# Kernel tuning notes

Hardware: AMD Instinct MI355X
Metric: run time of the kernel (lower is better)

Reference implementation:

```python
import jax, jax.numpy as jnp
import numpy as np

# Module constants from Net.__init__
KS = (3, 8, 2)          # kernel_size per pseudo-coordinate dim
K = KS[0] * KS[1] * KS[2]  # 48 spline weight matrices per layer
DIM = 3
S = 2 ** DIM            # 8 nonzero degree-1 B-spline supports per edge
MAX_RADIUS = 4.5
N, E = 20000, 500000


def _glorot(key, shape):
    fan = shape[-2] + shape[-1]
    return jax.random.normal(key, shape, jnp.float32) * jnp.sqrt(2.0 / fan)


def setup_inputs() -> dict:
    key = jax.random.key(0)
    ks = jax.random.split(key, 12)
    x = jax.random.normal(ks[0], (N, 1), jnp.float32)
    edge_index = jax.random.randint(ks[1], (2, E), 0, N)
    # raw pseudo-coordinates in [0, max_radius); normalized inside reference
    pseudo = jax.random.uniform(ks[2], (E, DIM), jnp.float32) * MAX_RADIUS
    return {
        "x": x,
        "edge_index": edge_index,
        "pseudo": pseudo,
        "W1": _glorot(ks[3], (K, 1, 32)),   "root1": _glorot(ks[4], (1, 32)),   "b1": jnp.zeros((32,), jnp.float32),
        "W2": _glorot(ks[5], (K, 32, 64)),  "root2": _glorot(ks[6], (32, 64)),  "b2": jnp.zeros((64,), jnp.float32),
        "W3": _glorot(ks[7], (K, 64, 128)), "root3": _glorot(ks[8], (64, 128)), "b3": jnp.zeros((128,), jnp.float32),
    }


def spline_basis(u):
    """Degree-1 open B-spline basis. u: [E, DIM] in [0,1].
    Returns basis [E, S] and flat kernel indices kidx [E, S] into the K weights."""
    ks_f = jnp.array(KS, jnp.float32)
    pos = u * (ks_f - 1.0)                      # [E, DIM]
    lo = jnp.floor(pos)
    frac = pos - lo                             # interpolation weight per dim
    lo_i = lo.astype(jnp.int32)
    # all 2^DIM corner offsets
    bits = jnp.array([[(s >> d) & 1 for d in range(DIM)] for s in range(S)], jnp.int32)  # [S, DIM]
    idx = jnp.clip(lo_i[:, None, :] + bits[None, :, :], 0, jnp.array(KS, jnp.int32) - 1)  # [E, S, DIM]
    w = jnp.where(bits[None, :, :] == 1, frac[:, None, :], 1.0 - frac[:, None, :])        # [E, S, DIM]
    basis = jnp.prod(w, axis=-1)                # [E, S]
    strides = jnp.array([KS[1] * KS[2], KS[2], 1], jnp.int32)
    kidx = (idx * strides[None, None, :]).sum(-1)  # [E, S]
    return basis, kidx


def spline_conv(x, src, dst, basis, kidx, W, root, bias):
    """SplineGCN layer: gather source features, weight by spline basis,
    scatter-add into per-(node, kernel) buckets, then contract with the K
    kernel matrices. Equivalent to sum_e basis * (x_src @ W[kidx]) at dst."""
    c_in = x.shape[1]
    contrib = basis[:, :, None] * x[src][:, None, :]          # [E, S, c_in]
    flat = (dst[:, None] * K + kidx).reshape(-1)              # [E*S]
    acc = jax.ops.segment_sum(contrib.reshape(-1, c_in), flat, num_segments=N * K)
    acc = acc.reshape(N, K, c_in)                             # [N, K, c_in]
    return jnp.einsum('nki,kio->no', acc, W) + x @ root + bias


def reference(x, edge_index, pseudo, W1, root1, b1, W2, root2, b2, W3, root3, b3):
    u = jnp.clip(pseudo / MAX_RADIUS, 0.0, 1.0)
    basis, kidx = spline_basis(u)
    src, dst = edge_index[0], edge_index[1]
    h = jax.nn.relu(spline_conv(x, src, dst, basis, kidx, W1, root1, b1))
    h = jax.nn.relu(spline_conv(h, src, dst, basis, kidx, W2, root2, b2))
    h = jax.nn.relu(spline_conv(h, src, dst, basis, kidx, W3, root3, b3))
    return jax.nn.log_softmax(h, axis=-1)
```

## Files before the change

kernel.cpp:

```cpp
#include <hip/hip_runtime.h>
#include <hip/hip_bf16.h>

#define NN_NODES 20000
#define NE_EDGES 500000
#define KTOT 48

typedef __bf16 bf16x8 __attribute__((ext_vector_type(8)));
typedef float f32x4 __attribute__((ext_vector_type(4)));

__device__ inline unsigned short bf16_rne(float x) {
    unsigned int u = __float_as_uint(x);
    u = (u + 0x7fffu + ((u >> 16) & 1u)) >> 16;
    return (unsigned short)u;
}

__global__ void zero_kernel(int* __restrict__ p, int n) {
    int i = blockIdx.x * 256 + threadIdx.x;
    if (i < n) p[i] = 0;
}

__global__ void count_kernel(const int* __restrict__ ei, int* __restrict__ counts) {
    int e = blockIdx.x * 256 + threadIdx.x;
    if (e < NE_EDGES) atomicAdd(&counts[ei[NE_EDGES + e]], 1);
}

__global__ void scan_kernel(const int* __restrict__ counts, int* __restrict__ row_start) {
    __shared__ int part[256];
    const int CH = (NN_NODES + 255) / 256;
    int t = threadIdx.x;
    int begin = t * CH;
    int end = begin + CH;
    if (end > NN_NODES) end = NN_NODES;
    int sum = 0;
    for (int i = begin; i < end && i < NN_NODES; ++i) sum += counts[i];
    part[t] = sum;
    __syncthreads();
    for (int off = 1; off < 256; off <<= 1) {
        int v = (t >= off) ? part[t - off] : 0;
        __syncthreads();
        part[t] += v;
        __syncthreads();
    }
    int run = (t == 0) ? 0 : part[t - 1];
    for (int i = begin; i < end && i < NN_NODES; ++i) {
        row_start[i] = run;
        run += counts[i];
    }
    if (t == 255) row_start[NN_NODES] = part[255];
}

__global__ void fill_kernel(const int* __restrict__ ei, const int* __restrict__ row_start,
                            int* __restrict__ cursor, int* __restrict__ slot_pos) {
    int e = blockIdx.x * 256 + threadIdx.x;
    if (e < NE_EDGES) {
        int d = ei[NE_EDGES + e];
        int p = atomicAdd(&cursor[d], 1);
        slot_pos[e] = row_start[d] + p;
    }
}

__global__ void edge_prep_sorted(const float* __restrict__ pseudo, const int* __restrict__ ei,
                                 const int* __restrict__ slot_pos,
                                 int* __restrict__ srcs,
                                 float* __restrict__ bas8, unsigned char* __restrict__ kidb) {
    int e = blockIdx.x * 256 + threadIdx.x;
    if (e >= NE_EDGES) return;
    const int ksa[3] = {3, 8, 2};
    float frac[3];
    int id_lo[3], id_hi[3];
#pragma unroll
    for (int d = 0; d < 3; ++d) {
        float u = pseudo[e * 3 + d] * (1.0f / 4.5f);
        u = fminf(fmaxf(u, 0.0f), 1.0f);
        float pos = u * (float)(ksa[d] - 1);
        float fl = floorf(pos);
        int lo = (int)fl;
        frac[d] = pos - fl;
        id_lo[d] = lo;
        id_hi[d] = (lo + 1 <= ksa[d] - 1) ? lo + 1 : lo - 1;
    }
    int j = slot_pos[e];
    srcs[j] = ei[e];
#pragma unroll
    for (int s = 0; s < 8; ++s) {
        float w = 1.0f;
        int k = 0;
        const int strides[3] = {16, 2, 1};
#pragma unroll
        for (int d = 0; d < 3; ++d) {
            int bit = (s >> d) & 1;
            k += (bit ? id_hi[d] : id_lo[d]) * strides[d];
            w *= bit ? frac[d] : (1.0f - frac[d]);
        }
        bas8[(size_t)j * 8 + s] = w;
        kidb[(size_t)j * 8 + s] = (unsigned char)k;
    }
}

__global__ __launch_bounds__(256) void layer1_fused_kernel(
    const int* __restrict__ srcs, const float* __restrict__ bas8,
    const unsigned char* __restrict__ kidb, const int* __restrict__ row_start,
    const float* __restrict__ x, const float* __restrict__ W1,
    const float* __restrict__ root1, const float* __restrict__ b1,
    unsigned short* __restrict__ h1bf) {
    __shared__ float w1s[KTOT * 32];
    __shared__ float scopy[4][8 * 49];
    int tid = threadIdx.x;
    for (int l = tid; l < KTOT * 32; l += 256) w1s[l] = W1[l];
    int w = tid >> 6, lane = tid & 63;
    int n = blockIdx.x * 4 + w;
    bool act = n < NN_NODES;
    float* sc = &scopy[w][0];
    for (int l = lane; l < 8 * 49; l += 64) sc[l] = 0.0f;
    if (act) {
        int beg = row_start[n], end = row_start[n + 1];
        int es = lane >> 3;
        for (int jb = beg; jb < end; jb += 8) {
            int j = jb + es;
            if (j < end) {
                float b = bas8[(size_t)jb * 8 + lane];
                int k = kidb[(size_t)jb * 8 + lane];
                float xv = x[srcs[j]];
                sc[es * 49 + k] += b * xv;
            }
        }
        if (lane < KTOT) {
            float a = 0.0f;
#pragma unroll
            for (int e = 0; e < 8; ++e) a += sc[e * 49 + lane];
            sc[lane] = a;
        }
    }
    __syncthreads();
    if (act && lane < 32) {
        float s = b1[lane] + x[n] * root1[lane];
#pragma unroll 8
        for (int k = 0; k < KTOT; ++k) s = fmaf(sc[k], w1s[k * 32 + lane], s);
        h1bf[n * 32 + lane] = bf16_rne(fmaxf(s, 0.0f));
    }
}

#define BTSTRIDE 40
template <int CIN>
__global__ __launch_bounds__(256) void mfma_acc_kernel(
    const int* __restrict__ srcs, const float* __restrict__ bas8,
    const unsigned char* __restrict__ kidb, const int* __restrict__ row_start,
    const unsigned short* __restrict__ hbf, unsigned short* __restrict__ abuf,
    int n0, int mc) {
    constexpr int NT = CIN / 16;
    __shared__ unsigned short BtAll[4][KTOT * BTSTRIDE];
    int w = threadIdx.x >> 6, lane = threadIdx.x & 63;
    int n_local = blockIdx.x * 4 + w;
    if (n_local >= mc) return;
    int n = n0 + n_local;
    unsigned short* Bt = &BtAll[w][0];
    int q = lane >> 4;
    int l15 = lane & 15;
    int beg = row_start[n], end = row_start[n + 1];
    int cnt = end - beg;
    f32x4 acc[3][NT] = {};

    for (int c0 = 0; c0 < cnt; c0 += 32) {
        uint4 z = make_uint4(0, 0, 0, 0);
        for (int l = lane; l < (KTOT * BTSTRIDE) / 8; l += 64) ((uint4*)Bt)[l] = z;
#pragma unroll
        for (int it = 0; it < 4; ++it) {
            int idx = it * 64 + lane;
            int jj = idx >> 3, s = idx & 7;
            int j = c0 + jj;
            if (j < cnt) {
                float b = bas8[(size_t)(beg + j) * 8 + s];
                int k = kidb[(size_t)(beg + j) * 8 + s];
                Bt[k * BTSTRIDE + jj] = bf16_rne(b);
            }
        }
        int srcv[8];
#pragma unroll
        for (int j = 0; j < 8; ++j) {
            int jc = c0 + q * 8 + j;
            jc = (jc < cnt) ? jc : (cnt - 1);
            srcv[j] = srcs[beg + jc];
        }
        bf16x8 afr[3];
#pragma unroll
        for (int mt = 0; mt < 3; ++mt) {
            uint4 raw = *(const uint4*)&Bt[(mt * 16 + l15) * BTSTRIDE + q * 8];
            afr[mt] = __builtin_bit_cast(bf16x8, raw);
        }
#pragma unroll
        for (int nt = 0; nt < NT; ++nt) {
            unsigned int bw[4];
#pragma unroll
            for (int jp = 0; jp < 4; ++jp) {
                unsigned int lo = hbf[(size_t)srcv[2 * jp] * CIN + nt * 16 + l15];
                unsigned int hi = hbf[(size_t)srcv[2 * jp + 1] * CIN + nt * 16 + l15];
                bw[jp] = lo | (hi << 16);
            }
            uint4 braw = make_uint4(bw[0], bw[1], bw[2], bw[3]);
            bf16x8 bfr = __builtin_bit_cast(bf16x8, braw);
#pragma unroll
            for (int mt = 0; mt < 3; ++mt)
                acc[mt][nt] = __builtin_amdgcn_mfma_f32_16x16x32_bf16(afr[mt], bfr,
                                                                      acc[mt][nt], 0, 0, 0);
        }
    }

    unsigned short* arow = abuf + (size_t)n_local * (49 * CIN);
#pragma unroll
    for (int mt = 0; mt < 3; ++mt)
#pragma unroll
        for (int nt = 0; nt < NT; ++nt)
#pragma unroll
            for (int r = 0; r < 4; ++r) {
                int kk = mt * 16 + q * 4 + r;
                int ch = nt * 16 + l15;
                arow[kk * CIN + ch] = bf16_rne(acc[mt][nt][r]);
            }
    if (lane < CIN) arow[KTOT * CIN + lane] = hbf[(size_t)n * CIN + lane];
}

__global__ void pack_w_kernel(const float* __restrict__ W, const float* __restrict__ root,
                              int KK, int NN, int total, unsigned short* __restrict__ Wp) {
    int tid = blockIdx.x * 256 + threadIdx.x;
    if (tid >= total) return;
    int nct = NN >> 4;
    int l = tid & 63;
    int c = (tid >> 6) % nct;
    int t = tid / (64 * nct);
    int n = c * 16 + (l & 15);
    int kbase = t * 32 + ((l >> 4) << 3);
    unsigned short vals[8];
#pragma unroll
    for (int jj = 0; jj < 8; ++jj) {
        int k = kbase + jj;
        float v = (k < KK) ? W[(size_t)k * NN + n] : root[(size_t)(k - KK) * NN + n];
        vals[jj] = bf16_rne(v);
    }
    *(uint4*)&Wp[(size_t)tid * 8] = *(uint4*)vals;
}

template <int NCT, int NW, bool LOGSOFTMAX>
__global__ __launch_bounds__(NW * 64) void mfma_gemm_block(
    const unsigned short* __restrict__ A, const unsigned short* __restrict__ Wp,
    const float* __restrict__ bias, void* __restrict__ outp,
    int Kp, int n0, int mc) {
    constexpr int NN = NCT * 16;
    constexpr int RSTR = NN + 2;
    __shared__ float red[NW][16 * RSTR];
    int w = threadIdx.x >> 6, lane = threadIdx.x & 63;
    int q = lane >> 4, l15 = lane & 15;
    int row_local = blockIdx.x * 16 + l15;
    int row_c = min(row_local, mc - 1);
    const unsigned short* arow = A + (size_t)row_c * Kp + (q << 3);
    const uint4* wpq = (const uint4*)Wp;
    f32x4 acc[NCT] = {};
    int tsteps = Kp >> 5;
    int t0 = (w * tsteps) / NW;
    int t1 = ((w + 1) * tsteps) / NW;

    uint4 na = *(const uint4*)(arow + t0 * 32);
    uint4 nb[NCT];
    {
        const uint4* bb = wpq + ((size_t)t0 * NCT) * 64 + lane;
#pragma unroll
        for (int c = 0; c < NCT; ++c) nb[c] = bb[c * 64];
    }
    for (int t = t0; t < t1; ++t) {
        uint4 ca = na;
        uint4 cb[NCT];
#pragma unroll
        for (int c = 0; c < NCT; ++c) cb[c] = nb[c];
        int tn = (t + 1 < t1) ? t + 1 : t;
        na = *(const uint4*)(arow + tn * 32);
        const uint4* bb = wpq + ((size_t)tn * NCT) * 64 + lane;
#pragma unroll
        for (int c = 0; c < NCT; ++c) nb[c] = bb[c * 64];
        bf16x8 af = __builtin_bit_cast(bf16x8, ca);
#pragma unroll
        for (int c = 0; c < NCT; ++c) {
            bf16x8 bfr = __builtin_bit_cast(bf16x8, cb[c]);
            acc[c] = __builtin_amdgcn_mfma_f32_16x16x32_bf16(af, bfr, acc[c], 0, 0, 0);
        }
    }

    float* myred = &red[w][0];
#pragma unroll
    for (int c = 0; c < NCT; ++c)
#pragma unroll
        for (int r = 0; r < 4; ++r)
            myred[(q * 4 + r) * RSTR + c * 16 + l15] = acc[c][r];
    __syncthreads();

    if (!LOGSOFTMAX) {
        unsigned short* outb = (unsigned short*)outp;
        for (int l = threadIdx.x; l < 16 * NN; l += NW * 64) {
            int row = l / NN, col = l % NN;
            int idx = row * RSTR + col;
            float v = 0.0f;
#pragma unroll
            for (int i = 0; i < NW; ++i) v += red[i][idx];
            v = fmaxf(v + bias[col], 0.0f);
            int ro = blockIdx.x * 16 + row;
            if (ro < mc) outb[(size_t)(n0 + ro) * NN + col] = bf16_rne(v);
        }
    } else {
        if (threadIdx.x < 256) {
            float* outf = (float*)outp;
            int row = threadIdx.x >> 4;
            int cb0 = threadIdx.x & 15;
            float v[8];
            float mx = -1e30f;
#pragma unroll
            for (int c = 0; c < 8; ++c) {
                int col = cb0 + c * 16;
                int idx = row * RSTR + col;
                float s = 0.0f;
#pragma unroll
                for (int i = 0; i < NW; ++i) s += red[i][idx];
                s = fmaxf(s + bias[col], 0.0f);
                v[c] = s;
                mx = fmaxf(mx, s);
            }
#pragma unroll
            for (int off = 8; off > 0; off >>= 1) mx = fmaxf(mx, __shfl_xor(mx, off));
            float se = 0.0f;
#pragma unroll
            for (int c = 0; c < 8; ++c) se += expf(v[c] - mx);
#pragma unroll
            for (int off = 8; off > 0; off >>= 1) se += __shfl_xor(se, off);
            float lse = mx + logf(se);
            int ro = blockIdx.x * 16 + row;
            if (ro < mc) {
#pragma unroll
                for (int c = 0; c < 8; ++c)
                    outf[(size_t)(n0 + ro) * 128 + cb0 + c * 16] = v[c] - lse;
            }
        }
    }
}

extern "C" void kernel_launch(void* const* d_in, const int* in_sizes, int n_in,
                              void* d_out, int out_size, void* d_ws, size_t ws_size,
                              hipStream_t stream) {
    const float* x = (const float*)d_in[0];
    const int* ei = (const int*)d_in[1];
    const float* pseudo = (const float*)d_in[2];
    const float* W1 = (const float*)d_in[3];
    const float* root1 = (const float*)d_in[4];
    const float* b1 = (const float*)d_in[5];
    const float* W2 = (const float*)d_in[6];
    const float* root2 = (const float*)d_in[7];
    const float* b2 = (const float*)d_in[8];
    const float* W3 = (const float*)d_in[9];
    const float* root3 = (const float*)d_in[10];
    const float* b3 = (const float*)d_in[11];
    float* out = (float*)d_out;
    char* ws = (char*)d_ws;

    const int N = NN_NODES, E = NE_EDGES;
    const int Kp2 = 49 * 32;
    const int Kp3 = 49 * 64;
    size_t off = 0;
    auto carve = [&](size_t bytes) {
        size_t p = off;
        off += (bytes + 255) & ~(size_t)255;
        return p;
    };
    int* counts = (int*)(ws + carve((size_t)N * 4 * 2));
    int* cursor = counts + N;
    int* row_start = (int*)(ws + carve((size_t)(N + 1) * 4));
    int* slot_pos = (int*)(ws + carve((size_t)E * 4));
    int* srcs = (int*)(ws + carve((size_t)E * 4));
    float* bas8 = (float*)(ws + carve((size_t)E * 8 * 4));
    unsigned char* kidb = (unsigned char*)(ws + carve((size_t)E * 8));
    unsigned short* h1bf = (unsigned short*)(ws + carve((size_t)N * 32 * 2));
    unsigned short* h2bf = (unsigned short*)(ws + carve((size_t)N * 64 * 2));
    unsigned short* Wp2 = (unsigned short*)(ws + carve((size_t)Kp2 * 64 * 2));
    unsigned short* Wp3 = (unsigned short*)(ws + carve((size_t)Kp3 * 128 * 2));
    size_t rem = (ws_size > off) ? (ws_size - off) : 0;
    unsigned short* abuf = (unsigned short*)(ws + off);

    int ch2 = (int)(rem / ((size_t)Kp2 * 2));
    int ch3 = (int)(rem / ((size_t)Kp3 * 2));
    if (ch2 > N) ch2 = N;
    if (ch3 > N) ch3 = N;
    if (ch2 < 1) ch2 = 1;
    if (ch3 < 1) ch3 = 1;

    int egrid = (E + 255) / 256;

    zero_kernel<<<(2 * N + 255) / 256, 256, 0, stream>>>(counts, 2 * N);
    count_kernel<<<egrid, 256, 0, stream>>>(ei, counts);
    scan_kernel<<<1, 256, 0, stream>>>(counts, row_start);
    fill_kernel<<<egrid, 256, 0, stream>>>(ei, row_start, cursor, slot_pos);
    edge_prep_sorted<<<egrid, 256, 0, stream>>>(pseudo, ei, slot_pos, srcs, bas8, kidb);

    int tot2 = (Kp2 / 32) * (64 / 16) * 64;
    int tot3 = (Kp3 / 32) * (128 / 16) * 64;
    pack_w_kernel<<<(tot2 + 255) / 256, 256, 0, stream>>>(W2, root2, KTOT * 32, 64, tot2, Wp2);
    pack_w_kernel<<<(tot3 + 255) / 256, 256, 0, stream>>>(W3, root3, KTOT * 64, 128, tot3, Wp3);

    layer1_fused_kernel<<<(N + 3) / 4, 256, 0, stream>>>(srcs, bas8, kidb, row_start, x,
                                                         W1, root1, b1, h1bf);

    for (int n0 = 0; n0 < N; n0 += ch2) {
        int mc = N - n0 < ch2 ? N - n0 : ch2;
        mfma_acc_kernel<32><<<(mc + 3) / 4, 256, 0, stream>>>(
            srcs, bas8, kidb, row_start, h1bf, abuf, n0, mc);
        mfma_gemm_block<4, 4, false><<<(mc + 15) / 16, 256, 0, stream>>>(
            abuf, Wp2, b2, h2bf, Kp2, n0, mc);
    }

    for (int n0 = 0; n0 < N; n0 += ch3) {
        int mc = N - n0 < ch3 ? N - n0 : ch3;
        mfma_acc_kernel<64><<<(mc + 3) / 4, 256, 0, stream>>>(
            srcs, bas8, kidb, row_start, h2bf, abuf, n0, mc);
        mfma_gemm_block<8, 8, true><<<(mc + 15) / 16, 512, 0, stream>>>(
            abuf, Wp3, b3, out, Kp3, n0, mc);
    }
}
```

Before: 346.6 us.

## Fuse layer-3 per-node spline aggregation with the weight GEMM and log-softmax

Replaces the two-kernel layer-3 path, which wrote a bf16 [N, K*64+64] accumulation buffer to global memory and then read it back for the GEMM, with a single kernel. Each 512-thread block handles 16 nodes, builds their aggregated rows in shared memory using MFMA over edge chunks, then runs the 16x3136x128 GEMM and log-softmax in place. This removes a large global write and read and one launch per chunk. In exchange it needs heavy shared memory per block, which lowers occupancy, and it assumes N is a multiple of 16.

Result: faster. 324.8 us (-6.3%).

```diff
diff --git a/kernel.cpp b/kernel.cpp
--- a/kernel.cpp
+++ b/kernel.cpp
@@ -239,10 +239,10 @@
     *(uint4*)&Wp[(size_t)tid * 8] = *(uint4*)vals;
 }
 
-template <int NCT, int NW, bool LOGSOFTMAX>
+template <int NCT, int NW>
 __global__ __launch_bounds__(NW * 64) void mfma_gemm_block(
     const unsigned short* __restrict__ A, const unsigned short* __restrict__ Wp,
-    const float* __restrict__ bias, void* __restrict__ outp,
+    const float* __restrict__ bias, unsigned short* __restrict__ outb,
     int Kp, int n0, int mc) {
     constexpr int NN = NCT * 16;
     constexpr int RSTR = NN + 2;
@@ -291,51 +291,135 @@
             myred[(q * 4 + r) * RSTR + c * 16 + l15] = acc[c][r];
     __syncthreads();
 
-    if (!LOGSOFTMAX) {
-        unsigned short* outb = (unsigned short*)outp;
-        for (int l = threadIdx.x; l < 16 * NN; l += NW * 64) {
-            int row = l / NN, col = l % NN;
-            int idx = row * RSTR + col;
-            float v = 0.0f;
-#pragma unroll
-            for (int i = 0; i < NW; ++i) v += red[i][idx];
-            v = fmaxf(v + bias[col], 0.0f);
-            int ro = blockIdx.x * 16 + row;
-            if (ro < mc) outb[(size_t)(n0 + ro) * NN + col] = bf16_rne(v);
-        }
-    } else {
-        if (threadIdx.x < 256) {
-            float* outf = (float*)outp;
-            int row = threadIdx.x >> 4;
-            int cb0 = threadIdx.x & 15;
-            float v[8];
-            float mx = -1e30f;
-#pragma unroll
-            for (int c = 0; c < 8; ++c) {
-                int col = cb0 + c * 16;
-                int idx = row * RSTR + col;
-                float s = 0.0f;
-#pragma unroll
-                for (int i = 0; i < NW; ++i) s += red[i][idx];
-                s = fmaxf(s + bias[col], 0.0f);
-                v[c] = s;
-                mx = fmaxf(mx, s);
-            }
-#pragma unroll
-            for (int off = 8; off > 0; off >>= 1) mx = fmaxf(mx, __shfl_xor(mx, off));
-            float se = 0.0f;
-#pragma unroll
-            for (int c = 0; c < 8; ++c) se += expf(v[c] - mx);
-#pragma unroll
-            for (int off = 8; off > 0; off >>= 1) se += __shfl_xor(se, off);
-            float lse = mx + logf(se);
-            int ro = blockIdx.x * 16 + row;
-            if (ro < mc) {
-#pragma unroll
-                for (int c = 0; c < 8; ++c)
-                    outf[(size_t)(n0 + ro) * 128 + cb0 + c * 16] = v[c] - lse;
-            }
-        }
+    for (int l = threadIdx.x; l < 16 * NN; l += NW * 64) {
+        int row = l / NN, col = l % NN;
+        int idx = row * RSTR + col;
+        float v = 0.0f;
+#pragma unroll
+        for (int i = 0; i < NW; ++i) v += red[i][idx];
+        v = fmaxf(v + bias[col], 0.0f);
+        int ro = blockIdx.x * 16 + row;
+        if (ro < mc) outb[(size_t)(n0 + ro) * NN + col] = bf16_rne(v);
+    }
+}
+
+#define ASTR 3152
+__global__ __launch_bounds__(512) void fused_l3_kernel(
+    const int* __restrict__ srcs, const float* __restrict__ bas8,
+    const unsigned char* __restrict__ kidb, const int* __restrict__ row_start,
+    const unsigned short* __restrict__ h2bf, const unsigned short* __restrict__ Wp3,
+    const float* __restrict__ b3, float* __restrict__ out) {
+    __shared__ unsigned short Arows[16 * ASTR];
+    __shared__ unsigned short BtAll[8][KTOT * BTSTRIDE];
+    float* Cst = (float*)&BtAll[0][0];
+    int w = threadIdx.x >> 6, lane = threadIdx.x & 63;
+    int q = lane >> 4, l15 = lane & 15;
+    unsigned short* Bt = &BtAll[w][0];
+
+    for (int u = 0; u < 2; ++u) {
+        int slot = w * 2 + u;
+        int n = blockIdx.x * 16 + slot;
+        int beg = row_start[n], end = row_start[n + 1];
+        int cnt = end - beg;
+        f32x4 acc[3][4] = {};
+        for (int c0 = 0; c0 < cnt; c0 += 32) {
+            uint4 z = make_uint4(0, 0, 0, 0);
+            for (int l = lane; l < (KTOT * BTSTRIDE) / 8; l += 64) ((uint4*)Bt)[l] = z;
+#pragma unroll
+            for (int it = 0; it < 4; ++it) {
+                int idx = it * 64 + lane;
+                int jj = idx >> 3, s = idx & 7;
+                int j = c0 + jj;
+                if (j < cnt) {
+                    float b = bas8[(size_t)(beg + j) * 8 + s];
+                    int k = kidb[(size_t)(beg + j) * 8 + s];
+                    Bt[k * BTSTRIDE + jj] = bf16_rne(b);
+                }
+            }
+            int srcv[8];
+#pragma unroll
+            for (int j = 0; j < 8; ++j) {
+                int jc = c0 + q * 8 + j;
+                jc = (jc < cnt) ? jc : (cnt - 1);
+                srcv[j] = srcs[beg + jc];
+            }
+            bf16x8 afr[3];
+#pragma unroll
+            for (int mt = 0; mt < 3; ++mt) {
+                uint4 raw = *(const uint4*)&Bt[(mt * 16 + l15) * BTSTRIDE + q * 8];
+                afr[mt] = __builtin_bit_cast(bf16x8, raw);
+            }
+#pragma unroll
+            for (int nt = 0; nt < 4; ++nt) {
+                unsigned int bw[4];
+#pragma unroll
+                for (int jp = 0; jp < 4; ++jp) {
+                    unsigned int lo = h2bf[(size_t)srcv[2 * jp] * 64 + nt * 16 + l15];
+                    unsigned int hi = h2bf[(size_t)srcv[2 * jp + 1] * 64 + nt * 16 + l15];
+                    bw[jp] = lo | (hi << 16);
+                }
+                uint4 braw = make_uint4(bw[0], bw[1], bw[2], bw[3]);
+                bf16x8 bfr = __builtin_bit_cast(bf16x8, braw);
+#pragma unroll
+                for (int mt = 0; mt < 3; ++mt)
+                    acc[mt][nt] = __builtin_amdgcn_mfma_f32_16x16x32_bf16(
+                        afr[mt], bfr, acc[mt][nt], 0, 0, 0);
+            }
+        }
+        unsigned short* arow = &Arows[slot * ASTR];
+#pragma unroll
+        for (int mt = 0; mt < 3; ++mt)
+#pragma unroll
+            for (int nt = 0; nt < 4; ++nt)
+#pragma unroll
+                for (int r = 0; r < 4; ++r)
+                    arow[(mt * 16 + q * 4 + r) * 64 + nt * 16 + l15] =
+                        bf16_rne(acc[mt][nt][r]);
+        arow[3072 + lane] = h2bf[(size_t)n * 64 + lane];
+    }
+    __syncthreads();
+
+    f32x4 cacc = {};
+    const uint4* wpq = (const uint4*)Wp3;
+    uint4 nb = wpq[(size_t)w * 64 + lane];
+    for (int t = 0; t < 98; ++t) {
+        uint4 cb = nb;
+        int tn = (t + 1 < 98) ? t + 1 : t;
+        nb = wpq[((size_t)tn * 8 + w) * 64 + lane];
+        bf16x8 af = __builtin_bit_cast(
+            bf16x8, *(const uint4*)&Arows[l15 * ASTR + t * 32 + (q << 3)]);
+        bf16x8 bfr = __builtin_bit_cast(bf16x8, cb);
+        cacc = __builtin_amdgcn_mfma_f32_16x16x32_bf16(af, bfr, cacc, 0, 0, 0);
+    }
+#pragma unroll
+    for (int r = 0; r < 4; ++r)
+        Cst[(q * 4 + r) * 130 + w * 16 + l15] = cacc[r];
+    __syncthreads();
+
+    if (threadIdx.x < 256) {
+        int row = threadIdx.x >> 4;
+        int cb0 = threadIdx.x & 15;
+        float v[8];
+        float mx = -1e30f;
+#pragma unroll
+        for (int c = 0; c < 8; ++c) {
+            float s = Cst[row * 130 + cb0 + c * 16] + b3[cb0 + c * 16];
+            s = fmaxf(s, 0.0f);
+            v[c] = s;
+            mx = fmaxf(mx, s);
+        }
+#pragma unroll
+        for (int off = 8; off > 0; off >>= 1) mx = fmaxf(mx, __shfl_xor(mx, off));
+        float se = 0.0f;
+#pragma unroll
+        for (int c = 0; c < 8; ++c) se += expf(v[c] - mx);
+#pragma unroll
+        for (int off = 8; off > 0; off >>= 1) se += __shfl_xor(se, off);
+        float lse = mx + logf(se);
+        int n = blockIdx.x * 16 + row;
+#pragma unroll
+        for (int c = 0; c < 8; ++c)
+            out[(size_t)n * 128 + cb0 + c * 16] = v[c] - lse;
     }
 }
 
@@ -381,11 +465,8 @@
     unsigned short* abuf = (unsigned short*)(ws + off);
 
     int ch2 = (int)(rem / ((size_t)Kp2 * 2));
-    int ch3 = (int)(rem / ((size_t)Kp3 * 2));
     if (ch2 > N) ch2 = N;
-    if (ch3 > N) ch3 = N;
     if (ch2 < 1) ch2 = 1;
-    if (ch3 < 1) ch3 = 1;
 
     int egrid = (E + 255) / 256;
 
@@ -407,15 +488,10 @@
         int mc = N - n0 < ch2 ? N - n0 : ch2;
         mfma_acc_kernel<32><<<(mc + 3) / 4, 256, 0, stream>>>(
             srcs, bas8, kidb, row_start, h1bf, abuf, n0, mc);
-        mfma_gemm_block<4, 4, false><<<(mc + 15) / 16, 256, 0, stream>>>(
+        mfma_gemm_block<4, 4><<<(mc + 15) / 16, 256, 0, stream>>>(
             abuf, Wp2, b2, h2bf, Kp2, n0, mc);
     }
 
-    for (int n0 = 0; n0 < N; n0 += ch3) {
-        int mc = N - n0 < ch3 ? N - n0 : ch3;
-        mfma_acc_kernel<64><<<(mc + 3) / 4, 256, 0, stream>>>(
-            srcs, bas8, kidb, row_start, h2bf, abuf, n0, mc);
-        mfma_gemm_block<8, 8, true><<<(mc + 15) / 16, 512, 0, stream>>>(
-            abuf, Wp3, b3, out, Kp3, n0, mc);
-    }
-}
+    fused_l3_kernel<<<N / 16, 512, 0, stream>>>(srcs, bas8, kidb, row_start,
+                                                h2bf, Wp3, b3, out);
+}
```
